# Kernel optimization log

Measured on AMD Instinct MI355X. Metric: run time of the kernel, lower is better.

## Reference

```python
import jax, jax.numpy as jnp
import numpy as np
import math

B, M, C, H = 4, 2048, 512, 8
DQK = C // 4 // H  # 16 per-head query/key dim


def setup_inputs() -> dict:
    key = jax.random.key(0)
    ks = jax.random.split(key, 8)
    s = 0.02
    return {
        "x": jax.random.normal(ks[0], (B, M, C), dtype=jnp.float32),
        "mask": jax.random.randint(ks[1], (B, M), 0, 2, dtype=jnp.int32),
        "Wq": jax.random.normal(ks[2], (C, C // 4), dtype=jnp.float32) * s,
        "bq": jnp.zeros((C // 4,), dtype=jnp.float32),
        "Wk": jax.random.normal(ks[3], (C, C // 4), dtype=jnp.float32) * s,
        "bk": jnp.zeros((C // 4,), dtype=jnp.float32),
        "Wv": jax.random.normal(ks[4], (C, C), dtype=jnp.float32) * s,
        "bv": jnp.zeros((C,), dtype=jnp.float32),
        "gamma": jnp.ones((1,), dtype=jnp.float32),
    }


def reference(x, mask, Wq, bq, Wk, bk, Wv, bv, gamma):
    b, m, c = x.shape
    # projections, split heads: q/k -> (B, H, M, DQK), v -> (B, H, M, C//H)
    q = (x @ Wq + bq).reshape(b, m, H, -1).transpose(0, 2, 1, 3)
    k = (x @ Wk + bk).reshape(b, m, H, -1).transpose(0, 2, 1, 3)
    v = (x @ Wv + bv).reshape(b, m, H, -1).transpose(0, 2, 1, 3)
    scale = 1.0 / math.sqrt(q.shape[-1])
    scores = jnp.einsum('bhmd,bhnd->bhmn', q, k) * scale
    beta = jax.nn.softmax(jax.nn.relu(scores), axis=-1)  # act='relu' pre-softmax
    # att_drop = 0.0 -> identity
    mf = mask.astype(x.dtype)[:, None, None, :]  # (B,1,1,M)
    beta = beta * mf
    beta = beta / (beta.sum(-1, keepdims=True) + 1e-12)
    o = gamma * jnp.einsum('bhmn,bhnd->bhmd', beta, v)  # (B,H,M,C//H)
    return o.transpose(0, 2, 1, 3).reshape(b, m, c)
```

## Files before the change

kernel.cpp:

```cpp
#include <hip/hip_runtime.h>
#include <hip/hip_bf16.h>

#define MSEQ 2048

typedef __attribute__((ext_vector_type(8))) short short8;
typedef __attribute__((ext_vector_type(4))) short short4v;
typedef __attribute__((ext_vector_type(4))) float f32x4;

static __device__ __forceinline__ short bf16b(float f) {
    __hip_bfloat16 h = __float2bfloat16(f);
    return *reinterpret_cast<short*>(&h);
}

static __device__ __forceinline__ void gl_lds16(const void* g, void* l) {
    __builtin_amdgcn_global_load_lds(
        (const __attribute__((address_space(1))) unsigned int*)g,
        (__attribute__((address_space(3))) unsigned int*)l, 16, 0, 0);
}

__global__ __launch_bounds__(256) void xcvt_kernel(
    const float* __restrict__ x, unsigned short* __restrict__ xb)
{
    const size_t i = ((size_t)blockIdx.x * 256 + threadIdx.x) * 8;
    const float4 a = *(const float4*)(x + i);
    const float4 b = *(const float4*)(x + i + 4);
    short8 o;
    o[0]=bf16b(a.x); o[1]=bf16b(a.y); o[2]=bf16b(a.z); o[3]=bf16b(a.w);
    o[4]=bf16b(b.x); o[5]=bf16b(b.y); o[6]=bf16b(b.z); o[7]=bf16b(b.w);
    *(short8*)(xb + i) = o;
}

__global__ __launch_bounds__(256) void wtrans_kernel(
    const float* __restrict__ Wq, const float* __restrict__ Wk,
    const float* __restrict__ Wv, unsigned short* __restrict__ WT)
{
    const int nt = blockIdx.x;
    const int kt = blockIdx.y;
    const int t  = threadIdx.x;
    const int k0 = kt*64;

    const float* W; int ld, n0;
    if (nt < 2)      { W = Wq; ld = 128; n0 = nt*64; }
    else if (nt < 4) { W = Wk; ld = 128; n0 = (nt-2)*64; }
    else             { W = Wv; ld = 512; n0 = (nt-4)*64; }

    __shared__ unsigned short Ts[64*72];

    #pragma unroll
    for (int s = 0; s < 4; ++s) {
        const int lin = s*256 + t;
        const int krow = lin >> 4, ng = lin & 15;
        const float4 v = *(const float4*)(W + (size_t)(k0+krow)*ld + n0 + ng*4);
        Ts[(ng*4+0)*72 + krow] = (unsigned short)bf16b(v.x);
        Ts[(ng*4+1)*72 + krow] = (unsigned short)bf16b(v.y);
        Ts[(ng*4+2)*72 + krow] = (unsigned short)bf16b(v.z);
        Ts[(ng*4+3)*72 + krow] = (unsigned short)bf16b(v.w);
    }
    __syncthreads();
    #pragma unroll
    for (int s = 0; s < 2; ++s) {
        const int lin = s*256 + t;
        const int nrow = lin >> 3, kg = lin & 7;
        *(short8*)(WT + (size_t)(nt*64 + nrow)*512 + k0 + kg*8) = *(const short8*)&Ts[nrow*72 + kg*8];
    }
}

__global__ __launch_bounds__(256, 2) void proj_mfma(
    const unsigned short* __restrict__ xb, const unsigned short* __restrict__ WT,
    const float* __restrict__ bq, const float* __restrict__ bk, const float* __restrict__ bv,
    unsigned short* __restrict__ Qb, unsigned short* __restrict__ Kb, unsigned short* __restrict__ Vt)
{
    const int nt = blockIdx.x;
    const int r0 = blockIdx.y * 128;
    const int n0 = nt * 128;
    const int t = threadIdx.x, w = t >> 6, lane = t & 63, l15 = lane & 15, quad = lane >> 4;
    const int qh = w >> 1, chh = w & 1;

    __shared__ short smem[128*136];
    short* As = smem;
    short* Bs = smem + 128*32;

    f32x4 acc[4][4];
    #pragma unroll
    for (int i = 0; i < 4; ++i)
        #pragma unroll
        for (int j = 0; j < 4; ++j) acc[i][j] = {0.f,0.f,0.f,0.f};

    const int arow = lane >> 2, akg = lane & 3;

    for (int kk = 0; kk < 512; kk += 32) {
        #pragma unroll
        for (int s = 0; s < 2; ++s) {
            const int row = w*32 + s*16 + arow;
            gl_lds16(xb + (size_t)(r0+row)*512 + kk + akg*8, As + (w*32 + s*16)*32);
            gl_lds16(WT + (size_t)(n0+row)*512 + kk + akg*8, Bs + (w*32 + s*16)*32);
        }
        __syncthreads();
        short8 Af[4], Bf[4];
        #pragma unroll
        for (int i = 0; i < 4; ++i) Af[i] = *(const short8*)&As[(qh*64 + i*16 + l15)*32 + quad*8];
        #pragma unroll
        for (int j = 0; j < 4; ++j) Bf[j] = *(const short8*)&Bs[(chh*64 + j*16 + l15)*32 + quad*8];
        #pragma unroll
        for (int i = 0; i < 4; ++i)
            #pragma unroll
            for (int j = 0; j < 4; ++j)
                acc[i][j] = __builtin_amdgcn_mfma_f32_16x16x32_bf16(Af[i], Bf[j], acc[i][j], 0, 0, 0);
        __syncthreads();
    }

    const float* bias = (nt == 0) ? bq : (nt == 1) ? bk : (bv + (nt-2)*128);
    float bj[4];
    #pragma unroll
    for (int j = 0; j < 4; ++j) bj[j] = bias[chh*64 + j*16 + l15];

    short* Ts = smem;
    if (nt < 2) {
        #pragma unroll
        for (int i = 0; i < 4; ++i)
            #pragma unroll
            for (int j = 0; j < 4; ++j)
                #pragma unroll
                for (int r = 0; r < 4; ++r)
                    Ts[(qh*64 + i*16 + quad*4 + r)*136 + chh*64 + j*16 + l15] =
                        bf16b(acc[i][j][r] + bj[j]);
    } else {
        #pragma unroll
        for (int i = 0; i < 4; ++i)
            #pragma unroll
            for (int j = 0; j < 4; ++j)
                #pragma unroll
                for (int r = 0; r < 4; ++r)
                    Ts[(chh*64 + j*16 + l15)*136 + qh*64 + i*16 + quad*4 + r] =
                        bf16b(acc[i][j][r] + bj[j]);
    }
    __syncthreads();

    if (nt < 2) {
        unsigned short* Out = (nt == 0) ? Qb : Kb;
        #pragma unroll
        for (int s = 0; s < 8; ++s) {
            const int lin = s*256 + t, row = lin >> 4, seg = lin & 15;
            *(short8*)(Out + (size_t)(r0+row)*128 + seg*8) = *(const short8*)&Ts[row*136 + seg*8];
        }
    } else {
        const int b = r0 >> 11, key0 = r0 & 2047, chBase = (nt-2)*128;
        #pragma unroll
        for (int s = 0; s < 8; ++s) {
            const int lin = s*256 + t, row = lin >> 4, seg = lin & 15;
            *(short8*)(Vt + ((size_t)(b*512 + chBase + row))*MSEQ + key0 + seg*8) =
                *(const short8*)&Ts[row*136 + seg*8];
        }
    }
}

__global__ __launch_bounds__(256, 4) void attn_mfma(
    const unsigned short* __restrict__ Qb, const unsigned short* __restrict__ Kb,
    const unsigned short* __restrict__ Vt, const int* __restrict__ mask,
    const float* __restrict__ gamma, float* __restrict__ out)
{
    const int bh = blockIdx.x;
    const int b  = bh >> 3, h = bh & 7;
    const int m0 = blockIdx.y * 64;
    const int t  = threadIdx.x;
    const int wave = t >> 6, lane = t & 63, l15 = lane & 15, quad = lane >> 4;

    __shared__ short Ks[64*24];
    __shared__ short Qs[64*24];
    __shared__ short VtS[64*72];
    __shared__ short Ws[64*72];
    __shared__ float msk[64];
    __shared__ float wsl[4*64];
    __shared__ float wsums[64];

    if (t < 64) {
        short8 z = {0,0,0,0,0,0,0,0};
        *(short8*)&Ks[t*24 + 16] = z;
        *(short8*)&Qs[t*24 + 16] = z;
    }
    if (t < 128) {
        const int row = t >> 1, half = t & 1;
        *(short8*)&Qs[row*24 + half*8] =
            *(const short8*)(Qb + (size_t)(b*MSEQ + m0 + row)*128 + h*16 + half*8);
    }
    __syncthreads();

    const int kso = (quad < 2) ? quad*8 : 16;
    short8 qfrag[4];
    #pragma unroll
    for (int c = 0; c < 4; ++c)
        qfrag[c] = *(const short8*)&Qs[(c*16 + l15)*24 + kso];

    f32x4 acc[2][2] = {{{0.f,0.f,0.f,0.f},{0.f,0.f,0.f,0.f}},
                       {{0.f,0.f,0.f,0.f},{0.f,0.f,0.f,0.f}}};
    float wsum_acc[4] = {0.f,0.f,0.f,0.f};
    const int qh = wave >> 1, chh = wave & 1;

    for (int kt = 0; kt < 32; ++kt) {
        const int kn0 = kt*64;
        if (t < 128) {
            const int key = t >> 1, half = t & 1;
            *(short8*)&Ks[key*24 + half*8] =
                *(const short8*)(Kb + (size_t)(b*MSEQ + kn0 + key)*128 + h*16 + half*8);
        }
        #pragma unroll
        for (int i = 0; i < 2; ++i) {
            const int idx = i*256 + t;
            const int kg = idx & 7, ch = idx >> 3;
            *(short8*)&VtS[ch*72 + kg*8] =
                *(const short8*)(Vt + ((size_t)(b*512 + h*64 + ch))*MSEQ + kn0 + kg*8);
        }
        if (t < 64) msk[t] = (float)mask[b*MSEQ + kn0 + t];
        __syncthreads();

        const short8 kfrag = *(const short8*)&Ks[(wave*16 + l15)*24 + kso];
        const float4 mk4 = *(const float4*)&msk[wave*16 + quad*4];
        #pragma unroll
        for (int c = 0; c < 4; ++c) {
            f32x4 s = {0.f,0.f,0.f,0.f};
            s = __builtin_amdgcn_mfma_f32_16x16x32_bf16(kfrag, qfrag[c], s, 0, 0, 0);
            float w0 = mk4.x * __expf(fmaxf(0.25f*s[0], 0.f));
            float w1 = mk4.y * __expf(fmaxf(0.25f*s[1], 0.f));
            float w2 = mk4.z * __expf(fmaxf(0.25f*s[2], 0.f));
            float w3 = mk4.w * __expf(fmaxf(0.25f*s[3], 0.f));
            short4v ws4;
            ws4[0]=bf16b(w0); ws4[1]=bf16b(w1); ws4[2]=bf16b(w2); ws4[3]=bf16b(w3);
            *(short4v*)&Ws[(c*16 + l15)*72 + wave*16 + quad*4] = ws4;
            float tsum = (w0 + w1) + (w2 + w3);
            tsum += __shfl_xor(tsum, 16, 64);
            tsum += __shfl_xor(tsum, 32, 64);
            wsum_acc[c] += tsum;
        }
        __syncthreads();

        short8 Af[2][2], Bf[2][2];
        #pragma unroll
        for (int si = 0; si < 2; ++si)
            #pragma unroll
            for (int kh = 0; kh < 2; ++kh)
                Af[si][kh] = *(const short8*)&Ws[((qh*2+si)*16 + l15)*72 + kh*32 + quad*8];
        #pragma unroll
        for (int ci = 0; ci < 2; ++ci)
            #pragma unroll
            for (int kh = 0; kh < 2; ++kh)
                Bf[ci][kh] = *(const short8*)&VtS[((chh*2+ci)*16 + l15)*72 + kh*32 + quad*8];
        #pragma unroll
        for (int si = 0; si < 2; ++si)
            #pragma unroll
            for (int ci = 0; ci < 2; ++ci)
                #pragma unroll
                for (int kh = 0; kh < 2; ++kh)
                    acc[si][ci] = __builtin_amdgcn_mfma_f32_16x16x32_bf16(
                        Af[si][kh], Bf[ci][kh], acc[si][ci], 0, 0, 0);
        __syncthreads();
    }

    if (quad == 0) {
        #pragma unroll
        for (int c = 0; c < 4; ++c) wsl[wave*64 + c*16 + l15] = wsum_acc[c];
    }
    __syncthreads();
    if (t < 64) wsums[t] = (wsl[t] + wsl[64+t]) + (wsl[128+t] + wsl[192+t]);
    __syncthreads();

    const float g = gamma[0];
    #pragma unroll
    for (int si = 0; si < 2; ++si) {
        #pragma unroll
        for (int r = 0; r < 4; ++r) {
            const int row = qh*32 + si*16 + quad*4 + r;
            const float inv = g / fmaxf(wsums[row], 1e-20f);
            #pragma unroll
            for (int ci = 0; ci < 2; ++ci) {
                const int col = chh*32 + ci*16 + l15;
                out[(size_t)(b*MSEQ + m0 + row)*512 + h*64 + col] = acc[si][ci][r] * inv;
            }
        }
    }
}

extern "C" void kernel_launch(void* const* d_in, const int* in_sizes, int n_in,
                              void* d_out, int out_size, void* d_ws, size_t ws_size,
                              hipStream_t stream) {
    const float* x     = (const float*)d_in[0];
    const int*   mask  = (const int*)  d_in[1];
    const float* Wq    = (const float*)d_in[2];
    const float* bq    = (const float*)d_in[3];
    const float* Wk    = (const float*)d_in[4];
    const float* bk    = (const float*)d_in[5];
    const float* Wv    = (const float*)d_in[6];
    const float* bv    = (const float*)d_in[7];
    const float* gamma = (const float*)d_in[8];
    float* outp = (float*)d_out;

    unsigned short* xb = (unsigned short*)d_ws;
    unsigned short* WT = xb + (size_t)8192*512;
    unsigned short* Qb = WT + (size_t)768*512;
    unsigned short* Kb = Qb + (size_t)8192*128;
    unsigned short* Vt = Kb + (size_t)8192*128;

    xcvt_kernel<<<2048, 256, 0, stream>>>(x, xb);
    wtrans_kernel<<<dim3(12, 8), 256, 0, stream>>>(Wq, Wk, Wv, WT);
    proj_mfma<<<dim3(6, 64), 256, 0, stream>>>(xb, WT, bq, bk, bv, Qb, Kb, Vt);
    attn_mfma<<<dim3(32, 32), 256, 0, stream>>>(Qb, Kb, Vt, mask, gamma, outp);
}
```

Measured before the change: 169.1 us.

## Load Q/K/V fragments directly from global, double-buffer weights, drop LDS staging

Removes the LDS staging of Q, K, V^T and the mask. MFMA fragments are now loaded straight from global memory into registers, and the probability tile Ws is double-buffered so one of the two barriers per key tile can be dropped. The cross-lane shuffle reduction of row sums moves out of the loop to the end, exp is computed with exp2 on a prescaled argument, and the grid is reordered so query tiles vary fastest. The trade-off is more uncached-pattern global loads per wave (V rows strided by MSEQ), which rely on L2 for reuse instead of shared memory.

```diff
diff --git a/kernel.cpp b/kernel.cpp
--- a/kernel.cpp
+++ b/kernel.cpp
@@ -159,77 +159,55 @@
     const unsigned short* __restrict__ Vt, const int* __restrict__ mask,
     const float* __restrict__ gamma, float* __restrict__ out)
 {
-    const int bh = blockIdx.x;
+    const int m0 = blockIdx.x * 64;
+    const int bh = blockIdx.y;
     const int b  = bh >> 3, h = bh & 7;
-    const int m0 = blockIdx.y * 64;
     const int t  = threadIdx.x;
     const int wave = t >> 6, lane = t & 63, l15 = lane & 15, quad = lane >> 4;
-
-    __shared__ short Ks[64*24];
-    __shared__ short Qs[64*24];
-    __shared__ short VtS[64*72];
-    __shared__ short Ws[64*72];
-    __shared__ float msk[64];
+    const int qh = wave >> 1, chh = wave & 1;
+
+    __shared__ short Ws[2*64*68];
     __shared__ float wsl[4*64];
     __shared__ float wsums[64];
 
-    if (t < 64) {
-        short8 z = {0,0,0,0,0,0,0,0};
-        *(short8*)&Ks[t*24 + 16] = z;
-        *(short8*)&Qs[t*24 + 16] = z;
-    }
-    if (t < 128) {
-        const int row = t >> 1, half = t & 1;
-        *(short8*)&Qs[row*24 + half*8] =
-            *(const short8*)(Qb + (size_t)(b*MSEQ + m0 + row)*128 + h*16 + half*8);
-    }
-    __syncthreads();
-
-    const int kso = (quad < 2) ? quad*8 : 16;
+    const short8 zz = {0,0,0,0,0,0,0,0};
+
     short8 qfrag[4];
     #pragma unroll
     for (int c = 0; c < 4; ++c)
-        qfrag[c] = *(const short8*)&Qs[(c*16 + l15)*24 + kso];
+        qfrag[c] = (quad < 2)
+            ? *(const short8*)(Qb + (size_t)(b*MSEQ + m0 + c*16 + l15)*128 + h*16 + quad*8)
+            : zz;
 
     f32x4 acc[2][2] = {{{0.f,0.f,0.f,0.f},{0.f,0.f,0.f,0.f}},
                        {{0.f,0.f,0.f,0.f},{0.f,0.f,0.f,0.f}}};
     float wsum_acc[4] = {0.f,0.f,0.f,0.f};
-    const int qh = wave >> 1, chh = wave & 1;
+
+    const unsigned short* Vrow0 = Vt + ((size_t)(b*512 + h*64))*MSEQ;
+    constexpr float SC = 0.25f * 1.44269504f;
 
     for (int kt = 0; kt < 32; ++kt) {
         const int kn0 = kt*64;
-        if (t < 128) {
-            const int key = t >> 1, half = t & 1;
-            *(short8*)&Ks[key*24 + half*8] =
-                *(const short8*)(Kb + (size_t)(b*MSEQ + kn0 + key)*128 + h*16 + half*8);
-        }
-        #pragma unroll
-        for (int i = 0; i < 2; ++i) {
-            const int idx = i*256 + t;
-            const int kg = idx & 7, ch = idx >> 3;
-            *(short8*)&VtS[ch*72 + kg*8] =
-                *(const short8*)(Vt + ((size_t)(b*512 + h*64 + ch))*MSEQ + kn0 + kg*8);
-        }
-        if (t < 64) msk[t] = (float)mask[b*MSEQ + kn0 + t];
-        __syncthreads();
-
-        const short8 kfrag = *(const short8*)&Ks[(wave*16 + l15)*24 + kso];
-        const float4 mk4 = *(const float4*)&msk[wave*16 + quad*4];
+        short* Wp = Ws + (kt & 1)*64*68;
+
+        const short8 kfrag = (quad < 2)
+            ? *(const short8*)(Kb + (size_t)(b*MSEQ + kn0 + wave*16 + l15)*128 + h*16 + quad*8)
+            : zz;
+        const int4 mi = *(const int4*)(mask + b*MSEQ + kn0 + wave*16 + quad*4);
+        const float mk[4] = {(float)mi.x, (float)mi.y, (float)mi.z, (float)mi.w};
+
         #pragma unroll
         for (int c = 0; c < 4; ++c) {
             f32x4 s = {0.f,0.f,0.f,0.f};
             s = __builtin_amdgcn_mfma_f32_16x16x32_bf16(kfrag, qfrag[c], s, 0, 0, 0);
-            float w0 = mk4.x * __expf(fmaxf(0.25f*s[0], 0.f));
-            float w1 = mk4.y * __expf(fmaxf(0.25f*s[1], 0.f));
-            float w2 = mk4.z * __expf(fmaxf(0.25f*s[2], 0.f));
-            float w3 = mk4.w * __expf(fmaxf(0.25f*s[3], 0.f));
+            float w0 = mk[0] * exp2f(fmaxf(SC*s[0], 0.f));
+            float w1 = mk[1] * exp2f(fmaxf(SC*s[1], 0.f));
+            float w2 = mk[2] * exp2f(fmaxf(SC*s[2], 0.f));
+            float w3 = mk[3] * exp2f(fmaxf(SC*s[3], 0.f));
             short4v ws4;
             ws4[0]=bf16b(w0); ws4[1]=bf16b(w1); ws4[2]=bf16b(w2); ws4[3]=bf16b(w3);
-            *(short4v*)&Ws[(c*16 + l15)*72 + wave*16 + quad*4] = ws4;
-            float tsum = (w0 + w1) + (w2 + w3);
-            tsum += __shfl_xor(tsum, 16, 64);
-            tsum += __shfl_xor(tsum, 32, 64);
-            wsum_acc[c] += tsum;
+            *(short4v*)&Wp[(c*16 + l15)*68 + wave*16 + quad*4] = ws4;
+            wsum_acc[c] += (w0 + w1) + (w2 + w3);
         }
         __syncthreads();
 
@@ -238,12 +216,13 @@
         for (int si = 0; si < 2; ++si)
             #pragma unroll
             for (int kh = 0; kh < 2; ++kh)
-                Af[si][kh] = *(const short8*)&Ws[((qh*2+si)*16 + l15)*72 + kh*32 + quad*8];
+                Af[si][kh] = *(const short8*)&Wp[((qh*2+si)*16 + l15)*68 + kh*32 + quad*8];
         #pragma unroll
         for (int ci = 0; ci < 2; ++ci)
             #pragma unroll
             for (int kh = 0; kh < 2; ++kh)
-                Bf[ci][kh] = *(const short8*)&VtS[((chh*2+ci)*16 + l15)*72 + kh*32 + quad*8];
+                Bf[ci][kh] = *(const short8*)(Vrow0 + ((size_t)((chh*2+ci)*16 + l15))*MSEQ
+                                              + kn0 + kh*32 + quad*8);
         #pragma unroll
         for (int si = 0; si < 2; ++si)
             #pragma unroll
@@ -252,12 +231,14 @@
                 for (int kh = 0; kh < 2; ++kh)
                     acc[si][ci] = __builtin_amdgcn_mfma_f32_16x16x32_bf16(
                         Af[si][kh], Bf[ci][kh], acc[si][ci], 0, 0, 0);
-        __syncthreads();
-    }
-
-    if (quad == 0) {
-        #pragma unroll
-        for (int c = 0; c < 4; ++c) wsl[wave*64 + c*16 + l15] = wsum_acc[c];
+    }
+
+    #pragma unroll
+    for (int c = 0; c < 4; ++c) {
+        float v = wsum_acc[c];
+        v += __shfl_xor(v, 16, 64);
+        v += __shfl_xor(v, 32, 64);
+        if (quad == 0) wsl[wave*64 + c*16 + l15] = v;
     }
     __syncthreads();
     if (t < 64) wsums[t] = (wsl[t] + wsl[64+t]) + (wsl[128+t] + wsl[192+t]);
```

Measured after the change: 186.0 us. 1.1x slower.
